# Performance work log

Measured on AMD Instinct MI355X. Metric: run time of the kernel, lower is better.

Reference implementation:

```python
import jax, jax.numpy as jnp
import numpy as np

N, E, D, H, C, K = 100000, 1250000, 64, 64, 40, 2


def setup_inputs() -> dict:
    key = jax.random.key(0)
    ks = jax.random.split(key, 10)
    s_in = 1.0 / np.sqrt(D)
    s_cat = 1.0 / np.sqrt(H * (K + 1))
    return {
        "x": jax.random.normal(ks[0], (N, D), jnp.float32),
        "edge_index": jax.random.randint(ks[1], (2, E), 0, N, dtype=jnp.int64),
        "W_ego": jax.random.normal(ks[2], (D, H), jnp.float32) * s_in,
        "b_ego": jnp.zeros((H,), jnp.float32),
        "W_conv": jax.random.normal(ks[3], (K, D, H), jnp.float32) * s_in,
        "b_conv": jnp.zeros((K, H), jnp.float32),
        "W_cls": jax.random.normal(ks[4], (H * (K + 1), C), jnp.float32) * s_cat,
        "b_cls": jnp.zeros((C,), jnp.float32),
    }


def _gcn_norm(edge_index, n):
    # PyG GCNConv default: add self-loops, symmetric normalization.
    row = jnp.concatenate([edge_index[0], jnp.arange(n, dtype=edge_index.dtype)])
    col = jnp.concatenate([edge_index[1], jnp.arange(n, dtype=edge_index.dtype)])
    deg = jax.ops.segment_sum(jnp.ones_like(col, dtype=jnp.float32), col, num_segments=n)
    dis = jnp.where(deg > 0, jax.lax.rsqrt(jnp.maximum(deg, 1.0)), 0.0)
    norm = dis[row] * dis[col]  # [E+N]
    return row, col, norm


def _gcn_conv(h, W, b, row, col, norm, n):
    hw = h @ W                                   # [N, H] transform first (cheap d)
    msg = norm[:, None] * hw[row]                # gather + scale, [E+N, H]
    agg = jax.ops.segment_sum(msg, col, num_segments=n)  # scatter-add to targets
    return agg + b


def reference(x, edge_index, W_ego, b_ego, W_conv, b_conv, W_cls, b_cls):
    n = x.shape[0]
    row, col, norm = _gcn_norm(edge_index, n)
    parts = [jax.nn.relu(x @ W_ego + b_ego)]
    h = x
    for k in range(K):
        h = jax.nn.relu(_gcn_conv(h, W_conv[k], b_conv[k], row, col, norm, n))
        parts.append(h)
    out = jnp.concatenate(parts, axis=-1)        # [N, H*(K+1)]
    # dropout is identity at inference (training=False)
    return out @ W_cls + b_cls
```

## Files before the change

kernel.cpp:

```cpp
#include <hip/hip_runtime.h>

using u16 = unsigned short;
using u32 = unsigned int;
using short8 = __attribute__((ext_vector_type(8))) short;
using f32x4  = __attribute__((ext_vector_type(4))) float;

static inline int cdiv(long long a, long long b) { return (int)((a + b - 1) / b); }

__device__ __forceinline__ u16 f2bf(float x) {
    u32 u = __builtin_bit_cast(u32, x);
    u += 0x7fffu + ((u >> 16) & 1u);
    return (u16)(u >> 16);
}
__device__ __forceinline__ float bf2f(u16 h) {
    u32 u = ((u32)h) << 16;
    return __builtin_bit_cast(float, u);
}

#define BKT_SH 10
#define BKT_MASK ((1 << BKT_SH) - 1)
#define HCHUNK 8192
#define CHUNK 4096

__global__ __launch_bounds__(256) void k_init(const int* __restrict__ ei,
                                              int* __restrict__ bpart, int E, int NBH,
                                              const float* __restrict__ Wego,
                                              const float* __restrict__ Wconv,
                                              const float* __restrict__ Wcls,
                                              u16* __restrict__ WTin,
                                              u16* __restrict__ WT1,
                                              u16* __restrict__ WcatT) {
    if ((int)blockIdx.x < NBH) {
        __shared__ int lb[128];
        if (threadIdx.x < 128) lb[threadIdx.x] = 0;
        __syncthreads();
        const int eb = blockIdx.x * HCHUNK;
#pragma unroll
        for (int k = 0; k < 32; ++k) {
            int e = eb + k * 256 + threadIdx.x;
            if (e < E) atomicAdd(&lb[ei[E + e] >> BKT_SH], 1);
        }
        __syncthreads();
        if (threadIdx.x < 128)
            bpart[blockIdx.x * 128 + threadIdx.x] = lb[threadIdx.x];
    } else {
        int t = ((int)blockIdx.x - NBH) * 256 + threadIdx.x;
        if (t < 128 * 64) {
            int seg = t >> 6, d = t & 63;
            float v = (seg < 64) ? Wconv[d * 64 + seg] : Wego[d * 64 + (seg - 64)];
            WTin[t] = f2bf(v);
        } else if (t < 128 * 64 + 64 * 64) {
            int u = t - 128 * 64;
            int c = u >> 6, d = u & 63;
            WT1[u] = f2bf(Wconv[64 * 64 + d * 64 + c]);
        } else if (t < 128 * 64 + 64 * 64 + 48 * 192) {
            int u = t - (128 * 64 + 64 * 64);
            int c = u / 192, d = u - c * 192;
            WcatT[u] = f2bf(c < 40 ? Wcls[d * 40 + c] : 0.f);
        }
    }
}

__global__ __launch_bounds__(128) void k_bscan(const int* __restrict__ bpart, int NBH,
                                               int* __restrict__ bbase,
                                               int* __restrict__ bcursor, int NB) {
    __shared__ int s[128];
    int t = threadIdx.x;
    int c = 0;
    for (int b = 0; b < NBH; ++b) c += bpart[b * 128 + t];
    int v = (t < NB) ? c : 0;
    s[t] = v;
    __syncthreads();
    for (int st = 1; st < 128; st <<= 1) {
        int add = (t >= st) ? s[t - st] : 0;
        __syncthreads();
        s[t] += add;
        __syncthreads();
    }
    int excl = s[t] - v;
    if (t < NB) { bbase[t] = excl; bcursor[t] = excl; }
    if (t == NB - 1) bbase[NB] = excl + v;
}

__global__ __launch_bounds__(256) void k_passA(const int* __restrict__ ei,
                                               int* __restrict__ bcursor,
                                               u32* __restrict__ sta, int E) {
    __shared__ int lcnt[128];
    __shared__ int lcur[128];
    if (threadIdx.x < 128) lcnt[threadIdx.x] = 0;
    __syncthreads();
    const int eb = blockIdx.x * CHUNK;
    int er[16], ec[16];
#pragma unroll
    for (int k = 0; k < 16; ++k) {
        int e = eb + k * 256 + threadIdx.x;
        if (e < E) {
            er[k] = ei[e];
            ec[k] = ei[E + e];
            atomicAdd(&lcnt[ec[k] >> BKT_SH], 1);
        } else {
            ec[k] = -1;
        }
    }
    __syncthreads();
    if (threadIdx.x < 128)
        lcur[threadIdx.x] = lcnt[threadIdx.x] > 0
                          ? atomicAdd(&bcursor[threadIdx.x], lcnt[threadIdx.x]) : 0;
    __syncthreads();
#pragma unroll
    for (int k = 0; k < 16; ++k) {
        if (ec[k] >= 0) {
            int pos = atomicAdd(&lcur[ec[k] >> BKT_SH], 1);
            sta[pos] = ((u32)(ec[k] & BKT_MASK) << 17) | (u32)er[k];
        }
    }
}

__global__ __launch_bounds__(256) void k_passB(const u32* __restrict__ sta,
                                               const int* __restrict__ bbase,
                                               int* __restrict__ indptr,
                                               float* __restrict__ dis,
                                               int* __restrict__ rows,
                                               int N, int NB) {
    __shared__ int lcnt[1024];
    __shared__ int cur[1024];
    __shared__ int ps[256];
    const int b = blockIdx.x;
    const int t = threadIdx.x;
    const int base = b << BKT_SH;
    const int e0 = bbase[b], e1 = bbase[b + 1];

#pragma unroll
    for (int k = 0; k < 4; ++k) lcnt[k * 256 + t] = 0;
    __syncthreads();
    for (int e = e0 + t; e < e1; e += 256)
        atomicAdd(&lcnt[sta[e] >> 17], 1);
    __syncthreads();

    int a0 = lcnt[t * 4 + 0], a1 = lcnt[t * 4 + 1];
    int a2 = lcnt[t * 4 + 2], a3 = lcnt[t * 4 + 3];
    int sum = a0 + a1 + a2 + a3;
    ps[t] = sum;
    __syncthreads();
    for (int st = 1; st < 256; st <<= 1) {
        int add = (t >= st) ? ps[t - st] : 0;
        __syncthreads();
        ps[t] += add;
        __syncthreads();
    }
    int ex = e0 + ps[t] - sum;
    int exs[4] = {ex, ex + a0, ex + a0 + a1, ex + a0 + a1 + a2};
    int cnts[4] = {a0, a1, a2, a3};
#pragma unroll
    for (int k = 0; k < 4; ++k) {
        int j = t * 4 + k;
        cur[j] = exs[k];
        int node = base + j;
        if (node < N) {
            indptr[node] = exs[k];
            dis[node] = rsqrtf((float)cnts[k] + 1.0f);
        }
    }
    if (b == NB - 1 && t == 0) indptr[N] = bbase[NB];
    __syncthreads();

    for (int e = e0 + t; e < e1; e += 256) {
        u32 v = sta[e];
        int pos = atomicAdd(&cur[v >> 17], 1);
        rows[pos] = (int)(v & 0x1FFFF);
    }
}

__global__ __launch_bounds__(256) void k_in(const float* __restrict__ x,
                                            const u16* __restrict__ WTin,
                                            const float* __restrict__ dis,
                                            const float* __restrict__ bego,
                                            u16* __restrict__ hws1,
                                            u16* __restrict__ hall, int N) {
    const int wid = (blockIdx.x * 256 + threadIdx.x) >> 6;
    const int l = threadIdx.x & 63;
    if (wid * 16 >= N) return;
    const int lr = l & 15;
    const int lk = l >> 4;

    int r_ld = wid * 16 + lr;
    if (r_ld >= N) r_ld = N - 1;
    const float* xrow = x + (size_t)r_ld * 64 + lk * 8;
    float4 u0 = *(const float4*)(xrow);
    float4 u1 = *(const float4*)(xrow + 4);
    float4 u2 = *(const float4*)(xrow + 32);
    float4 u3 = *(const float4*)(xrow + 36);
    short8 a0, a1;
    a0[0] = (short)f2bf(u0.x); a0[1] = (short)f2bf(u0.y);
    a0[2] = (short)f2bf(u0.z); a0[3] = (short)f2bf(u0.w);
    a0[4] = (short)f2bf(u1.x); a0[5] = (short)f2bf(u1.y);
    a0[6] = (short)f2bf(u1.z); a0[7] = (short)f2bf(u1.w);
    a1[0] = (short)f2bf(u2.x); a1[1] = (short)f2bf(u2.y);
    a1[2] = (short)f2bf(u2.z); a1[3] = (short)f2bf(u2.w);
    a1[4] = (short)f2bf(u3.x); a1[5] = (short)f2bf(u3.y);
    a1[6] = (short)f2bf(u3.z); a1[7] = (short)f2bf(u3.w);

    float dvals[4];
#pragma unroll
    for (int rg = 0; rg < 4; ++rg) {
        int r = wid * 16 + lk * 4 + rg;
        dvals[rg] = dis[r < N ? r : N - 1];
    }

    for (int ct = 0; ct < 8; ++ct) {
        const u16* wrow = WTin + ((size_t)(ct * 16 + lr)) * 64 + lk * 8;
        short8 b0 = *(const short8*)wrow;
        short8 b1 = *(const short8*)(wrow + 32);
        f32x4 acc = {0.f, 0.f, 0.f, 0.f};
        acc = __builtin_amdgcn_mfma_f32_16x16x32_bf16(a0, b0, acc, 0, 0, 0);
        acc = __builtin_amdgcn_mfma_f32_16x16x32_bf16(a1, b1, acc, 0, 0, 0);
        const int col = ct * 16 + lr;
        if (col < 64) {
#pragma unroll
            for (int rg = 0; rg < 4; ++rg) {
                int r = wid * 16 + lk * 4 + rg;
                if (r < N) hws1[(size_t)r * 64 + col] = f2bf(dvals[rg] * acc[rg]);
            }
        } else {
            float be = bego[col - 64];
#pragma unroll
            for (int rg = 0; rg < 4; ++rg) {
                int r = wid * 16 + lk * 4 + rg;
                if (r < N) hall[(size_t)r * 192 + (col - 64)] = f2bf(fmaxf(acc[rg] + be, 0.f));
            }
        }
    }
}

__global__ __launch_bounds__(512) void k_gather(const int* __restrict__ indptr,
                                                const int* __restrict__ rows,
                                                const float* __restrict__ dis,
                                                const float* __restrict__ bconv,
                                                const u16* __restrict__ hws_in,
                                                u16* __restrict__ hdst, int N) {
    const int w = threadIdx.x >> 6;
    const int f = threadIdx.x & 63;
    const int i = blockIdx.x * 8 + w;
    if (i >= N) return;

    float acc = bf2f(hws_in[(size_t)i * 64 + f]);
    int p0 = __builtin_amdgcn_readfirstlane(indptr[i]);
    int p1 = __builtin_amdgcn_readfirstlane(indptr[i + 1]);
    int p = p0;
    for (; p + 8 <= p1; p += 8) {
        int r0 = rows[p + 0], r1 = rows[p + 1], r2 = rows[p + 2], r3 = rows[p + 3];
        int r4 = rows[p + 4], r5 = rows[p + 5], r6 = rows[p + 6], r7 = rows[p + 7];
        u16 v0 = hws_in[(size_t)r0 * 64 + f];
        u16 v1 = hws_in[(size_t)r1 * 64 + f];
        u16 v2 = hws_in[(size_t)r2 * 64 + f];
        u16 v3 = hws_in[(size_t)r3 * 64 + f];
        u16 v4 = hws_in[(size_t)r4 * 64 + f];
        u16 v5 = hws_in[(size_t)r5 * 64 + f];
        u16 v6 = hws_in[(size_t)r6 * 64 + f];
        u16 v7 = hws_in[(size_t)r7 * 64 + f];
        acc += ((bf2f(v0) + bf2f(v1)) + (bf2f(v2) + bf2f(v3))) +
               ((bf2f(v4) + bf2f(v5)) + (bf2f(v6) + bf2f(v7)));
    }
    for (; p + 4 <= p1; p += 4) {
        int r0 = rows[p + 0], r1 = rows[p + 1], r2 = rows[p + 2], r3 = rows[p + 3];
        u16 v0 = hws_in[(size_t)r0 * 64 + f];
        u16 v1 = hws_in[(size_t)r1 * 64 + f];
        u16 v2 = hws_in[(size_t)r2 * 64 + f];
        u16 v3 = hws_in[(size_t)r3 * 64 + f];
        acc += (bf2f(v0) + bf2f(v1)) + (bf2f(v2) + bf2f(v3));
    }
    for (; p < p1; ++p) acc += bf2f(hws_in[(size_t)rows[p] * 64 + f]);

    float hv = fmaxf(fmaf(dis[i], acc, bconv[f]), 0.0f);
    hdst[(size_t)i * 192 + f] = f2bf(hv);
}

__global__ __launch_bounds__(256) void k_next1(const u16* __restrict__ hall,
                                               const u16* __restrict__ WT1,
                                               const float* __restrict__ dis,
                                               u16* __restrict__ hws, int N) {
    const int wid = (blockIdx.x * 256 + threadIdx.x) >> 6;
    const int l = threadIdx.x & 63;
    if (wid * 16 >= N) return;
    const int lr = l & 15;
    const int lk = l >> 4;

    int r_ld = wid * 16 + lr;
    if (r_ld >= N) r_ld = N - 1;
    const u16* arow = hall + (size_t)r_ld * 192 + 64 + lk * 8;
    short8 a0 = *(const short8*)arow;
    short8 a1 = *(const short8*)(arow + 32);

    float dvals[4];
#pragma unroll
    for (int rg = 0; rg < 4; ++rg) {
        int r = wid * 16 + lk * 4 + rg;
        dvals[rg] = dis[r < N ? r : N - 1];
    }

    for (int ct = 0; ct < 4; ++ct) {
        const u16* wrow = WT1 + ((size_t)(ct * 16 + lr)) * 64 + lk * 8;
        short8 b0 = *(const short8*)wrow;
        short8 b1 = *(const short8*)(wrow + 32);
        f32x4 acc = {0.f, 0.f, 0.f, 0.f};
        acc = __builtin_amdgcn_mfma_f32_16x16x32_bf16(a0, b0, acc, 0, 0, 0);
        acc = __builtin_amdgcn_mfma_f32_16x16x32_bf16(a1, b1, acc, 0, 0, 0);
        const int col = ct * 16 + lr;
#pragma unroll
        for (int rg = 0; rg < 4; ++rg) {
            int r = wid * 16 + lk * 4 + rg;
            if (r < N) hws[(size_t)r * 64 + col] = f2bf(dvals[rg] * acc[rg]);
        }
    }
}

__global__ __launch_bounds__(256) void k_clsall(const u16* __restrict__ hall,
                                                const u16* __restrict__ WcatT,
                                                const float* __restrict__ bcls,
                                                float* __restrict__ out, int N) {
    const int wid = (blockIdx.x * 256 + threadIdx.x) >> 6;
    const int l = threadIdx.x & 63;
    if (wid * 16 >= N) return;
    const int lr = l & 15;
    const int lk = l >> 4;

    int r_ld = wid * 16 + lr;
    if (r_ld >= N) r_ld = N - 1;
    const u16* arow = hall + (size_t)r_ld * 192 + lk * 8;
    short8 a[6];
#pragma unroll
    for (int kt = 0; kt < 6; ++kt) a[kt] = *(const short8*)(arow + kt * 32);

    for (int ct = 0; ct < 3; ++ct) {
        const u16* brow = WcatT + ((size_t)(ct * 16 + lr)) * 192 + lk * 8;
        f32x4 acc = {0.f, 0.f, 0.f, 0.f};
#pragma unroll
        for (int kt = 0; kt < 6; ++kt) {
            short8 b = *(const short8*)(brow + kt * 32);
            acc = __builtin_amdgcn_mfma_f32_16x16x32_bf16(a[kt], b, acc, 0, 0, 0);
        }
        const int col = ct * 16 + lr;
        if (col < 40) {
            float bc = bcls[col];
#pragma unroll
            for (int rg = 0; rg < 4; ++rg) {
                int r = wid * 16 + lk * 4 + rg;
                if (r < N) out[(size_t)r * 40 + col] = bc + acc[rg];
            }
        }
    }
}

extern "C" void kernel_launch(void* const* d_in, const int* in_sizes, int n_in,
                              void* d_out, int out_size, void* d_ws, size_t ws_size,
                              hipStream_t stream) {
    const float* x     = (const float*)d_in[0];
    const int*   ei    = (const int*)d_in[1];
    const float* Wego  = (const float*)d_in[2];
    const float* bego  = (const float*)d_in[3];
    const float* Wconv = (const float*)d_in[4];
    const float* bconv = (const float*)d_in[5];
    const float* Wcls  = (const float*)d_in[6];
    const float* bcls  = (const float*)d_in[7];
    float* out = (float*)d_out;

    const int N = in_sizes[0] / 64;
    const int E = in_sizes[1] / 2;
    const int NB   = cdiv(N, 1 << BKT_SH);
    const int NBH  = cdiv(E, HCHUNK);
    const int NBA  = cdiv(E, CHUNK);

    u16* hall  = (u16*)d_ws;
    u32* sta   = (u32*)d_ws;
    u16* hws1  = hall + (size_t)N * 192;
    u16* hws2  = hws1 + (size_t)N * 64;
    u16* WTin  = hws2 + (size_t)N * 64;
    u16* WT1   = WTin + 128 * 64;
    u16* WcatT = WT1 + 64 * 64;
    float* dis = (float*)(WcatT + 48 * 192);
    int* indptr  = (int*)(dis + N);
    int* bbase   = indptr + N + 64;
    int* bcursor = bbase + 132;
    int* rows    = bcursor + 128;
    int* bpart   = rows + E;

    const int PREP_BLOCKS = cdiv(128 * 64 + 64 * 64 + 48 * 192, 256);
    k_init<<<NBH + PREP_BLOCKS, 256, 0, stream>>>(ei, bpart, E, NBH,
                                                  Wego, Wconv, Wcls, WTin, WT1, WcatT);
    k_bscan<<<1, 128, 0, stream>>>(bpart, NBH, bbase, bcursor, NB);
    k_passA<<<NBA, 256, 0, stream>>>(ei, bcursor, sta, E);
    k_passB<<<NB, 256, 0, stream>>>(sta, bbase, indptr, dis, rows, N, NB);

    k_in<<<cdiv(cdiv(N, 16), 4), 256, 0, stream>>>(x, WTin, dis, bego, hws1, hall, N);

    k_gather<<<cdiv(N, 8), 512, 0, stream>>>(indptr, rows, dis, bconv,
                                             hws1, hall + 64, N);
    k_next1<<<cdiv(cdiv(N, 16), 4), 256, 0, stream>>>(hall, WT1, dis, hws2, N);

    k_gather<<<cdiv(N, 8), 512, 0, stream>>>(indptr, rows, dis, bconv + 64,
                                             hws2, hall + 128, N);

    k_clsall<<<cdiv(cdiv(N, 16), 4), 256, 0, stream>>>(hall, WcatT, bcls, out, N);
}
```

Measured before the change: 223.5 us.

## Gather two bf16 features per lane with half-wave rows; parallelize bucket scan

The gather kernel now assigns 32 lanes per node, and each lane loads a u32 holding two bf16 features. A wave therefore handles two destination nodes, which halves the number of load instructions and doubles the in-flight row gathers per wave. The indptr loads no longer use readfirstlane because each wave covers two nodes. The bucket scan kernel now reduces the per-block partial counts with 1024 threads in 8 slices instead of one serial loop over 128 threads.

```diff
diff --git a/kernel.cpp b/kernel.cpp
--- a/kernel.cpp
+++ b/kernel.cpp
@@ -15,6 +15,12 @@
 __device__ __forceinline__ float bf2f(u16 h) {
     u32 u = ((u32)h) << 16;
     return __builtin_bit_cast(float, u);
+}
+__device__ __forceinline__ float bflo(u32 v) {
+    return __builtin_bit_cast(float, v << 16);
+}
+__device__ __forceinline__ float bfhi(u32 v) {
+    return __builtin_bit_cast(float, v & 0xffff0000u);
 }
 
 #define BKT_SH 10
@@ -61,25 +67,37 @@
     }
 }
 
-__global__ __launch_bounds__(128) void k_bscan(const int* __restrict__ bpart, int NBH,
-                                               int* __restrict__ bbase,
-                                               int* __restrict__ bcursor, int NB) {
+__global__ __launch_bounds__(1024) void k_bscan(const int* __restrict__ bpart, int NBH,
+                                                int* __restrict__ bbase,
+                                                int* __restrict__ bcursor, int NB) {
+    __shared__ int part[8][128];
     __shared__ int s[128];
-    int t = threadIdx.x;
+    const int t = threadIdx.x;
+    const int bucket = t & 127, slice = t >> 7;
     int c = 0;
-    for (int b = 0; b < NBH; ++b) c += bpart[b * 128 + t];
-    int v = (t < NB) ? c : 0;
-    s[t] = v;
+    for (int b = slice; b < NBH; b += 8) c += bpart[b * 128 + bucket];
+    part[slice][bucket] = c;
+    __syncthreads();
+    int v = 0;
+    if (t < 128) {
+#pragma unroll
+        for (int k = 0; k < 8; ++k) v += part[k][t];
+        if (t >= NB) v = 0;
+        s[t] = v;
+    }
     __syncthreads();
     for (int st = 1; st < 128; st <<= 1) {
-        int add = (t >= st) ? s[t - st] : 0;
-        __syncthreads();
-        s[t] += add;
-        __syncthreads();
-    }
-    int excl = s[t] - v;
-    if (t < NB) { bbase[t] = excl; bcursor[t] = excl; }
-    if (t == NB - 1) bbase[NB] = excl + v;
+        int add = (t >= st && t < 128) ? s[t - st] : 0;
+        __syncthreads();
+        if (t < 128) s[t] += add;
+        __syncthreads();
+    }
+    if (t < NB) {
+        int excl = s[t] - v;
+        bbase[t] = excl;
+        bcursor[t] = excl;
+        if (t == NB - 1) bbase[NB] = s[t];
+    }
 }
 
 __global__ __launch_bounds__(256) void k_passA(const int* __restrict__ ei,
@@ -238,41 +256,53 @@
                                                 const float* __restrict__ bconv,
                                                 const u16* __restrict__ hws_in,
                                                 u16* __restrict__ hdst, int N) {
-    const int w = threadIdx.x >> 6;
-    const int f = threadIdx.x & 63;
-    const int i = blockIdx.x * 8 + w;
+    const int half = threadIdx.x >> 5;
+    const int c = threadIdx.x & 31;
+    const int i = blockIdx.x * 16 + half;
     if (i >= N) return;
 
-    float acc = bf2f(hws_in[(size_t)i * 64 + f]);
-    int p0 = __builtin_amdgcn_readfirstlane(indptr[i]);
-    int p1 = __builtin_amdgcn_readfirstlane(indptr[i + 1]);
+    const u32* src = (const u32*)hws_in;
+    u32 sv = src[(size_t)i * 32 + c];
+    float a0 = bflo(sv), a1 = bfhi(sv);
+
+    int p0 = indptr[i], p1 = indptr[i + 1];
     int p = p0;
     for (; p + 8 <= p1; p += 8) {
         int r0 = rows[p + 0], r1 = rows[p + 1], r2 = rows[p + 2], r3 = rows[p + 3];
         int r4 = rows[p + 4], r5 = rows[p + 5], r6 = rows[p + 6], r7 = rows[p + 7];
-        u16 v0 = hws_in[(size_t)r0 * 64 + f];
-        u16 v1 = hws_in[(size_t)r1 * 64 + f];
-        u16 v2 = hws_in[(size_t)r2 * 64 + f];
-        u16 v3 = hws_in[(size_t)r3 * 64 + f];
-        u16 v4 = hws_in[(size_t)r4 * 64 + f];
-        u16 v5 = hws_in[(size_t)r5 * 64 + f];
-        u16 v6 = hws_in[(size_t)r6 * 64 + f];
-        u16 v7 = hws_in[(size_t)r7 * 64 + f];
-        acc += ((bf2f(v0) + bf2f(v1)) + (bf2f(v2) + bf2f(v3))) +
-               ((bf2f(v4) + bf2f(v5)) + (bf2f(v6) + bf2f(v7)));
+        u32 v0 = src[(size_t)r0 * 32 + c];
+        u32 v1 = src[(size_t)r1 * 32 + c];
+        u32 v2 = src[(size_t)r2 * 32 + c];
+        u32 v3 = src[(size_t)r3 * 32 + c];
+        u32 v4 = src[(size_t)r4 * 32 + c];
+        u32 v5 = src[(size_t)r5 * 32 + c];
+        u32 v6 = src[(size_t)r6 * 32 + c];
+        u32 v7 = src[(size_t)r7 * 32 + c];
+        a0 += ((bflo(v0) + bflo(v1)) + (bflo(v2) + bflo(v3))) +
+              ((bflo(v4) + bflo(v5)) + (bflo(v6) + bflo(v7)));
+        a1 += ((bfhi(v0) + bfhi(v1)) + (bfhi(v2) + bfhi(v3))) +
+              ((bfhi(v4) + bfhi(v5)) + (bfhi(v6) + bfhi(v7)));
     }
     for (; p + 4 <= p1; p += 4) {
         int r0 = rows[p + 0], r1 = rows[p + 1], r2 = rows[p + 2], r3 = rows[p + 3];
-        u16 v0 = hws_in[(size_t)r0 * 64 + f];
-        u16 v1 = hws_in[(size_t)r1 * 64 + f];
-        u16 v2 = hws_in[(size_t)r2 * 64 + f];
-        u16 v3 = hws_in[(size_t)r3 * 64 + f];
-        acc += (bf2f(v0) + bf2f(v1)) + (bf2f(v2) + bf2f(v3));
-    }
-    for (; p < p1; ++p) acc += bf2f(hws_in[(size_t)rows[p] * 64 + f]);
-
-    float hv = fmaxf(fmaf(dis[i], acc, bconv[f]), 0.0f);
-    hdst[(size_t)i * 192 + f] = f2bf(hv);
+        u32 v0 = src[(size_t)r0 * 32 + c];
+        u32 v1 = src[(size_t)r1 * 32 + c];
+        u32 v2 = src[(size_t)r2 * 32 + c];
+        u32 v3 = src[(size_t)r3 * 32 + c];
+        a0 += (bflo(v0) + bflo(v1)) + (bflo(v2) + bflo(v3));
+        a1 += (bfhi(v0) + bfhi(v1)) + (bfhi(v2) + bfhi(v3));
+    }
+    for (; p < p1; ++p) {
+        u32 v = src[(size_t)rows[p] * 32 + c];
+        a0 += bflo(v);
+        a1 += bfhi(v);
+    }
+
+    float dsi = dis[i];
+    float2 bb = *(const float2*)(bconv + 2 * c);
+    float h0 = fmaxf(fmaf(dsi, a0, bb.x), 0.0f);
+    float h1 = fmaxf(fmaf(dsi, a1, bb.y), 0.0f);
+    ((u32*)hdst)[(size_t)i * 96 + c] = (u32)f2bf(h0) | ((u32)f2bf(h1) << 16);
 }
 
 __global__ __launch_bounds__(256) void k_next1(const u16* __restrict__ hall,
@@ -387,18 +417,18 @@
     const int PREP_BLOCKS = cdiv(128 * 64 + 64 * 64 + 48 * 192, 256);
     k_init<<<NBH + PREP_BLOCKS, 256, 0, stream>>>(ei, bpart, E, NBH,
                                                   Wego, Wconv, Wcls, WTin, WT1, WcatT);
-    k_bscan<<<1, 128, 0, stream>>>(bpart, NBH, bbase, bcursor, NB);
+    k_bscan<<<1, 1024, 0, stream>>>(bpart, NBH, bbase, bcursor, NB);
     k_passA<<<NBA, 256, 0, stream>>>(ei, bcursor, sta, E);
     k_passB<<<NB, 256, 0, stream>>>(sta, bbase, indptr, dis, rows, N, NB);
 
     k_in<<<cdiv(cdiv(N, 16), 4), 256, 0, stream>>>(x, WTin, dis, bego, hws1, hall, N);
 
-    k_gather<<<cdiv(N, 8), 512, 0, stream>>>(indptr, rows, dis, bconv,
-                                             hws1, hall + 64, N);
+    k_gather<<<cdiv(N, 16), 512, 0, stream>>>(indptr, rows, dis, bconv,
+                                              hws1, hall + 64, N);
     k_next1<<<cdiv(cdiv(N, 16), 4), 256, 0, stream>>>(hall, WT1, dis, hws2, N);
 
-    k_gather<<<cdiv(N, 8), 512, 0, stream>>>(indptr, rows, dis, bconv + 64,
-                                             hws2, hall + 128, N);
+    k_gather<<<cdiv(N, 16), 512, 0, stream>>>(indptr, rows, dis, bconv + 64,
+                                              hws2, hall + 128, N);
 
     k_clsall<<<cdiv(cdiv(N, 16), 4), 256, 0, stream>>>(hall, WcatT, bcls, out, N);
 }
```

After: 197.4 us (median of 2 runs). -11.7%, faster.
